# Optimization experiments

Measured on AMD Instinct MI355X. Metric: run time of the kernel, lower is better.

## Reference

```python
import jax, jax.numpy as jnp
import numpy as np

B, N, H, DK, DV = 2, 2048, 16, 128, 128
E = H * DV
EPS = 1e-6


def setup_inputs() -> dict:
    key = jax.random.key(0)
    ks = jax.random.split(key, 8)
    sc_qk = 1.0 / np.sqrt(E + H * DK)  # xavier_normal-ish std
    sc_e = 1.0 / np.sqrt(2 * E)
    d = {
        "x": jax.random.normal(ks[0], (B, N, E), jnp.float32),
        "Wq": jax.random.normal(ks[1], (H * DK, E), jnp.float32) * sc_qk,
        "bq": jnp.zeros((H * DK,), jnp.float32),
        "Wk": jax.random.normal(ks[2], (H * DK, E), jnp.float32) * sc_qk,
        "bk": jnp.zeros((H * DK,), jnp.float32),
        "Wv": jax.random.normal(ks[3], (E, E), jnp.float32) * sc_e,
        "bv": jnp.zeros((E,), jnp.float32),
        "Wg": jax.random.normal(ks[4], (E, E), jnp.float32) * sc_e,
        "bg": jnp.zeros((E,), jnp.float32),
        "Wo": jax.random.normal(ks[5], (E, E), jnp.float32) * sc_e,
        "bo": jnp.zeros((E,), jnp.float32),
        "start_idx": 0,
    }
    return d


def _retention_scan(q, k, v, decays):
    # q,k: [B,N,H,DK] (k already scaled), v: [B,N,H,DV]
    qs = jnp.moveaxis(q, 1, 0)  # [N,B,H,DK]
    ks_ = jnp.moveaxis(k, 1, 0)
    vs = jnp.moveaxis(v, 1, 0)
    dec = decays[None, :, None, None]  # [1,H,1,1]

    def step(state, qkv):
        qt, kt, vt = qkv
        # state_n = decay * state_{n-1} + k_n (x) v_n
        state = dec * state + kt[..., :, None] * vt[..., None, :]  # [B,H,DK,DV]
        ret = jnp.einsum("bhk,bhkv->bhv", qt, state)
        return state, ret

    init = jnp.zeros((q.shape[0], H, DK, DV), q.dtype)
    final_state, rets = jax.lax.scan(step, init, (qs, ks_, vs))
    return jnp.moveaxis(rets, 0, 1), final_state  # [B,N,H,DV], [B,H,DK,DV]


def reference(x, Wq, bq, Wk, bk, Wv, bv, Wg, bg, Wo, bo, start_idx):
    b, n, _ = x.shape
    decays = 1.0 - jnp.exp2(-5.0 - jnp.arange(H, dtype=jnp.float32))  # [H]
    q = (x @ Wq.T + bq).reshape(b, n, H, DK)
    k = (x @ Wk.T + bk).reshape(b, n, H, DK) / (DK ** 0.5)
    v = (x @ Wv.T + bv).reshape(b, n, H, DV)
    retention, state = _retention_scan(q, k, v, decays)
    # GroupNorm over (b n) tokens, num_groups=H, channels=E, no affine
    r = retention.reshape(b * n, H, DV).astype(jnp.float32)
    mu = jnp.mean(r, axis=-1, keepdims=True)
    var = jnp.var(r, axis=-1, keepdims=True)
    r = (r - mu) / jnp.sqrt(var + EPS)
    r = r.reshape(b, n, E).astype(x.dtype)
    gate = jax.nn.silu(x @ Wg.T + bg)
    out = (r * gate) @ Wo.T + bo
    return out, state
```

## Files before the change

kernel.cpp:

```cpp
#include <hip/hip_runtime.h>
#include <hip/hip_bf16.h>

typedef __attribute__((ext_vector_type(8))) short short8;
typedef __attribute__((ext_vector_type(4))) short short4v;
typedef __attribute__((ext_vector_type(4))) float floatx4;

#define DI __device__ __forceinline__

constexpr int B_ = 2, N_ = 2048, H_ = 16, DK_ = 128, DV_ = 128, E_ = 2048;
constexpr int M_ = B_ * N_;
constexpr int NCAT_ = 4 * E_;
constexpr int CH_ = 128;
constexpr int NC_ = N_ / CH_;
constexpr float KSCALE = 0.08838834764831845f;

constexpr long OFF_XB   = 0;
constexpr long OFF_WCAT = 16777216;
constexpr long OFF_WOB  = 50331648;
constexpr long OFF_BCAT = 58720256;
constexpr long OFF_Y    = 58753024;
constexpr long OFF_KT   = 125861888;
constexpr long OFF_VT   = 142639104;
constexpr long OFF_SCB  = 159416320;

DI unsigned short f2bf(float f){
  unsigned u = __float_as_uint(f);
  u += 0x7fffu + ((u >> 16) & 1u);
  return (unsigned short)(u >> 16);
}
DI float bf2f(unsigned short s){ return __uint_as_float(((unsigned)s) << 16); }

DI void gload_lds16(const void* g, void* l){
  __builtin_amdgcn_global_load_lds(
      (const __attribute__((address_space(1))) unsigned int*)g,
      (__attribute__((address_space(3))) unsigned int*)l, 16, 0, 0);
}

__global__ void k_cast(const float* __restrict__ s, unsigned short* __restrict__ d, int n){
  long i = ((long)blockIdx.x * blockDim.x + threadIdx.x) * 8;
  if(i >= n) return;
  float4 v0 = *(const float4*)(s + i);
  float4 v1 = *(const float4*)(s + i + 4);
  short8 o;
  o[0]=(short)f2bf(v0.x); o[1]=(short)f2bf(v0.y); o[2]=(short)f2bf(v0.z); o[3]=(short)f2bf(v0.w);
  o[4]=(short)f2bf(v1.x); o[5]=(short)f2bf(v1.y); o[6]=(short)f2bf(v1.z); o[7]=(short)f2bf(v1.w);
  *(short8*)(d + i) = o;
}

__global__ void k_bcat(const float* __restrict__ bq, const float* __restrict__ bk,
                       const float* __restrict__ bv, const float* __restrict__ bg,
                       float* __restrict__ bcat){
  int i = blockIdx.x * blockDim.x + threadIdx.x;
  float v;
  if(i < 2048)      v = bq[i];
  else if(i < 4096) v = bk[i - 2048];
  else if(i < 6144) v = bv[i - 4096];
  else              v = bg[i - 6144];
  bcat[i] = v;
}

__global__ __launch_bounds__(512, 2)
void k_gemm256(const unsigned short* __restrict__ A,
               const unsigned short* __restrict__ Bt,
               unsigned short* __restrict__ Y,
               const float* __restrict__ bias)
{
  extern __shared__ unsigned short lds[];
  constexpr int K = 2048;
  constexpr int NKT = K / 64;

  const int tid = threadIdx.x;
  const int wave = tid >> 6, lane = tid & 63;
  const int wr = wave >> 2, wc = wave & 3;
  const int l15 = lane & 15;

  int bid = blockIdx.x;
  int g = bid & 7, w = bid >> 3;
  int bm = (g & 1) * 8 + (w & 7);
  int bn = (g >> 1) * 8 + (w >> 3);

  const unsigned short* Ab = A  + (long)bm * 256 * K;
  const unsigned short* Bb = Bt + (long)bn * 256 * K;

  const int srow = wave * 8 + (lane >> 3);
  const int ce   = ((lane & 7) ^ ((lane >> 3) & 7)) * 8;

  const int colb[2] = { ((((lane >> 4))    ^ (lane & 7)) << 4),
                        ((((lane >> 4)+4)  ^ (lane & 7)) << 4) };
  int rbA[8], rbB[4];
  #pragma unroll
  for(int ai=0;ai<8;++ai) rbA[ai] = (ai>>2)*16384 + ((wr*64 + (ai&3)*16 + l15) << 7);
  #pragma unroll
  for(int bj=0;bj<4;++bj) rbB[bj] = (bj>>1)*16384 + ((wc*32 + (bj&1)*16 + l15) << 7);

  floatx4 acc[8][4] = {};
  const char* ldsc = (const char*)lds;

#define STG(op, buf, half, kt) do{                                                   \
    const unsigned short* _s = ((op) ? Bb : Ab) + (long)((half)*128 + srow)*K + (long)(kt)*64 + ce; \
    unsigned short* _d = lds + ((op)*32768 + (buf)*16384 + (half)*8192 + wave*512);  \
    gload_lds16(_s, _d);                                                             \
    gload_lds16(_s + 64*K, _d + 4096);                                               \
  }while(0)

  STG(0, 0, 0, 0);
  STG(1, 0, 0, 0);
  STG(0, 0, 1, 0);
  STG(1, 0, 1, 0);

  for(int u=0; u<NKT; ++u){
    const int cur = u & 1, nxt = cur ^ 1;
    const int ktn = (u + 1) & (NKT - 1);

    __syncthreads();

    STG(0, nxt, 0, ktn);
    STG(1, nxt, 0, ktn);
    STG(0, nxt, 1, ktn);
    STG(1, nxt, 1, ktn);

    const char* cA = ldsc + cur*32768;
    const char* cB = ldsc + 65536 + cur*32768;

    #pragma unroll
    for(int kk=0;kk<2;++kk){
      short8 a8[8], b4[4];
      #pragma unroll
      for(int ai=0;ai<8;++ai) a8[ai] = *(const short8*)(cA + rbA[ai] + colb[kk]);
      #pragma unroll
      for(int bj=0;bj<4;++bj) b4[bj] = *(const short8*)(cB + rbB[bj] + colb[kk]);
      #pragma unroll
      for(int ai=0;ai<8;++ai)
        #pragma unroll
        for(int bj=0;bj<4;++bj)
          acc[ai][bj] = __builtin_amdgcn_mfma_f32_16x16x32_bf16(a8[ai], b4[bj], acc[ai][bj], 0,0,0);
    }
  }
#undef STG

  #pragma unroll
  for(int ai=0;ai<8;++ai){
    const int rowi = bm*256 + (ai>>2)*128 + wr*64 + (ai&3)*16 + ((lane>>4)<<2);
    #pragma unroll
    for(int bj=0;bj<4;++bj){
      const int col = bn*256 + (bj>>1)*128 + wc*32 + (bj&1)*16 + l15;
      const float bs = bias[col];
      const int sec = col >> 11;
      #pragma unroll
      for(int r=0;r<4;++r){
        float v = acc[ai][bj][r] + bs;
        if(sec == 1) v *= KSCALE;
        else if(sec == 3) v = v / (1.f + __expf(-v));
        Y[(long)(rowi + r) * NCAT_ + col] = f2bf(v);
      }
    }
  }
}

template<int EPI>
__global__ __launch_bounds__(256)
void k_gemm(const unsigned short* __restrict__ A,
            const unsigned short* __restrict__ Bt,
            void* __restrict__ outp,
            const float* __restrict__ bias,
            int M, int Ncols, int K, int NB)
{
  __shared__ unsigned short lA[2*128*64];
  __shared__ unsigned short lB[2*128*64];
  const int bid = blockIdx.x;
  const int bm = bid / NB, bn = bid % NB;
  const int tid = threadIdx.x;
  const int wave = tid >> 6, lane = tid & 63;
  const int wr = wave >> 1, wc = wave & 1;

  floatx4 acc[4][4] = {};

  int srow[4], scol[4];
  #pragma unroll
  for(int is=0; is<4; ++is){
    int o = is*4096 + wave*1024 + lane*16;
    int row = o >> 7;
    int logcb = (o & 127) ^ ((row & 7) << 4);
    srow[is] = row; scol[is] = logcb >> 1;
  }
  const unsigned short* Abase = A + (long)bm * 128 * K;
  const unsigned short* Bbase = Bt + (long)bn * 128 * K;

#define STG128(kt, buf) do{                                                          \
    const int _k0 = (kt) << 6;                                                       \
    _Pragma("unroll")                                                                \
    for(int is=0; is<4; ++is){                                                       \
      gload_lds16(Abase + (long)srow[is]*K + _k0 + scol[is], &lA[(buf)*8192 + ((is*4096 + wave*1024) >> 1)]); \
      gload_lds16(Bbase + (long)srow[is]*K + _k0 + scol[is], &lB[(buf)*8192 + ((is*4096 + wave*1024) >> 1)]); \
    }                                                                                \
  }while(0)

  const int nkt = K >> 6;
  STG128(0, 0);
  for(int kt=0; kt<nkt; ++kt){
    const int cur = kt & 1, nxt = cur ^ 1;
    const int ktn = (kt + 1 == nkt) ? 0 : kt + 1;
    __syncthreads();
    STG128(ktn, nxt);
    const char* cA = (const char*)lA + cur*16384;
    const char* cB = (const char*)lB + cur*16384;
    #pragma unroll
    for(int kk=0; kk<2; ++kk){
      const int cb = (kk<<6) + ((lane>>4)<<4);
      short8 af[4], bfr[4];
      #pragma unroll
      for(int i=0;i<4;++i){
        int row = (wr<<6) + (i<<4) + (lane&15);
        af[i] = *(const short8*)(cA + (row<<7) + (cb ^ ((row&7)<<4)));
      }
      #pragma unroll
      for(int j=0;j<4;++j){
        int row = (wc<<6) + (j<<4) + (lane&15);
        bfr[j] = *(const short8*)(cB + (row<<7) + (cb ^ ((row&7)<<4)));
      }
      #pragma unroll
      for(int i=0;i<4;++i)
        #pragma unroll
        for(int j=0;j<4;++j)
          acc[i][j] = __builtin_amdgcn_mfma_f32_16x16x32_bf16(af[i], bfr[j], acc[i][j], 0,0,0);
    }
  }
#undef STG128

  #pragma unroll
  for(int i=0;i<4;++i){
    #pragma unroll
    for(int j=0;j<4;++j){
      #pragma unroll
      for(int r=0;r<4;++r){
        int row = bm*128 + (wr<<6) + (i<<4) + ((lane>>4)<<2) + r;
        int col = bn*128 + (wc<<6) + (j<<4) + (lane&15);
        float v = acc[i][j][r] + bias[col];
        if(EPI == 0){
          int sec = col >> 11;
          if(sec == 1) v *= KSCALE;
          else if(sec == 3) v = v / (1.f + __expf(-v));
          ((unsigned short*)outp)[(long)row * Ncols + col] = f2bf(v);
        } else {
          ((float*)outp)[(long)row * Ncols + col] = v;
        }
      }
    }
  }
}

__global__ __launch_bounds__(256)
void k_transpose(const unsigned short* __restrict__ Y,
                 unsigned short* __restrict__ Kt, unsigned short* __restrict__ Vt){
  __shared__ unsigned short lt[128][136];
  int bid = blockIdx.x;
  int op = bid >> 9;
  int r  = bid & 511;
  int bh = r >> 4, c = r & 15, b = bh >> 4, h = bh & 15;
  int tid = threadIdx.x;
  float dec = 1.f - exp2f(-5.f - (float)h);
  float l2d = log2f(dec);
  int sec = op ? 4096 : 2048;
  unsigned short* Dst = op ? Vt : Kt;

  #pragma unroll
  for(int p=0;p<8;++p){
    int t = p*16 + (tid>>4);
    long src = ((long)(b*N_ + c*CH_ + t)) * NCAT_ + sec + h*128 + (tid&15)*8;
    short8 v = *(const short8*)(Y + src);
    if(op == 0){
      float f = exp2f(-(float)t * l2d);
      #pragma unroll
      for(int u=0;u<8;++u) v[u] = (short)f2bf(bf2f((unsigned short)v[u]) * f);
    }
    *(short8*)&lt[t][(tid&15)*8] = v;
  }
  __syncthreads();
  #pragma unroll
  for(int p=0;p<8;++p){
    int dk = p*16 + (tid>>4);
    int tc = (tid&15)*8;
    short8 o;
    #pragma unroll
    for(int u=0;u<8;++u) o[u] = (short)lt[tc+u][dk];
    *(short8*)(Dst + ((long)(bh*128 + dk)) * N_ + c*CH_ + tc) = o;
  }
}

__global__ __launch_bounds__(256)
void k_chunksum(const unsigned short* __restrict__ Ktd, const unsigned short* __restrict__ Vt,
                float* __restrict__ MS){
  int bid = blockIdx.x;
  int bh = bid >> 4, c = bid & 15, h = bh & 15;
  int tid = threadIdx.x, wave = tid >> 6, lane = tid & 63;
  int wr = wave >> 1, wc = wave & 1;
  floatx4 acc[4][4] = {};
  const unsigned short* Vb = Vt  + (long)bh*128*N_ + c*CH_;
  const unsigned short* Kb = Ktd + (long)bh*128*N_ + c*CH_;

  #pragma unroll
  for(int kk=0;kk<4;++kk){
    int tl = kk*32 + ((lane>>4)<<3);
    short8 af[4], bfr[4];
    #pragma unroll
    for(int i=0;i<4;++i){ int dv = (wr<<6)+(i<<4)+(lane&15); af[i]  = *(const short8*)(Vb + (long)dv*N_ + tl); }
    #pragma unroll
    for(int j=0;j<4;++j){ int dk = (wc<<6)+(j<<4)+(lane&15); bfr[j] = *(const short8*)(Kb + (long)dk*N_ + tl); }
    #pragma unroll
    for(int i=0;i<4;++i)
      #pragma unroll
      for(int j=0;j<4;++j)
        acc[i][j] = __builtin_amdgcn_mfma_f32_16x16x32_bf16(af[i], bfr[j], acc[i][j], 0,0,0);
  }
  float dec = 1.f - exp2f(-5.f - (float)h);
  float scale = exp2f(127.f * log2f(dec));
  float* Mo = MS + ((long)bh*NC_ + c) * 16384;
  #pragma unroll
  for(int i=0;i<4;++i)
    #pragma unroll
    for(int j=0;j<4;++j)
      #pragma unroll
      for(int r=0;r<4;++r){
        int dv = (wr<<6)+(i<<4)+((lane>>4)<<2)+r;
        int dk = (wc<<6)+(j<<4)+(lane&15);
        Mo[dv*128 + dk] = acc[i][j][r] * scale;
      }
}

__global__ __launch_bounds__(256)
void k_scan(const float* __restrict__ MS, unsigned short* __restrict__ Scb,
            float* __restrict__ stateOut){
  int bid = blockIdx.x;
  int bh = bid >> 4, p = bid & 15;
  int tid = threadIdx.x, h = bh & 15;
  float dec = 1.f - exp2f(-5.f - (float)h);
  float decC = exp2f(128.f * log2f(dec));
  int e0 = p*1024 + tid*4;
  floatx4 S = {0.f, 0.f, 0.f, 0.f};
  const float* base = MS + (long)bh * NC_ * 16384 + e0;
  unsigned short* sb = Scb + (long)bh * NC_ * 16384 + e0;
  for(int c=0;c<NC_;++c){
    floatx4 m = *(const floatx4*)(base + (long)c*16384);
    short4v q;
    #pragma unroll
    for(int u=0;u<4;++u) q[u] = (short)f2bf(S[u]);
    *(short4v*)(sb + (long)c*16384) = q;
    S = decC * S + m;
  }
  int dv = e0 >> 7, dk = e0 & 127;
  float* so = stateOut + (long)bh*16384 + dv;
  #pragma unroll
  for(int u=0;u<4;++u) so[(long)(dk+u)*128] = S[u];
}

__global__ __launch_bounds__(256)
void k_ret(const unsigned short* __restrict__ Y, const unsigned short* __restrict__ Vt,
           const unsigned short* __restrict__ Scb, unsigned short* __restrict__ RG){
  __shared__ unsigned short sQ[128*128];
  __shared__ unsigned short sK[128*128];
  int bid = blockIdx.x;
  int bh = bid >> 4, c = bid & 15, b = bh >> 4, h = bh & 15;
  int tid = threadIdx.x, w = tid >> 6, lane = tid & 63;
  float dec = 1.f - exp2f(-5.f - (float)h);
  float l2d = log2f(dec);

  #pragma unroll
  for(int p=0;p<8;++p){
    int t = p*16 + (tid>>4);
    long row = (long)(b*N_ + c*CH_ + t) * NCAT_ + h*128 + (tid&15)*8;
    short8 qv = *(const short8*)(Y + row);
    short8 kv = *(const short8*)(Y + row + 2048);
    float fq = exp2f((float)t * l2d);
    float fk = exp2f(-(float)t * l2d);
    short8 qs, ks;
    #pragma unroll
    for(int u=0;u<8;++u){
      qs[u] = (short)f2bf(bf2f((unsigned short)qv[u]) * fq);
      ks[u] = (short)f2bf(bf2f((unsigned short)kv[u]) * fk);
    }
    int ad = t*256 + (((tid&15)*16) ^ ((t&7)<<4));
    *(short8*)((char*)sQ + ad) = qs;
    *(short8*)((char*)sK + ad) = ks;
  }
  __syncthreads();

  floatx4 acc[2][8] = {};
  #pragma unroll
  for(int kk=0;kk<4;++kk){
    int cb = (kk<<6) + ((lane>>4)<<4);
    short8 af[2], bfr[8];
    #pragma unroll
    for(int i=0;i<2;++i){ int t = w*32 + (i<<4) + (lane&15); af[i] = *(const short8*)((const char*)sQ + t*256 + (cb ^ ((t&7)<<4))); }
    #pragma unroll
    for(int j=0;j<8;++j){ int s = (j<<4) + (lane&15); bfr[j] = *(const short8*)((const char*)sK + s*256 + (cb ^ ((s&7)<<4))); }
    #pragma unroll
    for(int i=0;i<2;++i)
      #pragma unroll
      for(int j=0;j<8;++j)
        acc[i][j] = __builtin_amdgcn_mfma_f32_16x16x32_bf16(af[i], bfr[j], acc[i][j], 0,0,0);
  }
  __syncthreads();

  #pragma unroll
  for(int i=0;i<2;++i)
    #pragma unroll
    for(int j=0;j<8;++j)
      #pragma unroll
      for(int r=0;r<4;++r){
        int t = w*32 + (i<<4) + ((lane>>4)<<2) + r;
        int s = (j<<4) + (lane&15);
        float v = (s <= t) ? acc[i][j][r] : 0.f;
        *(unsigned short*)((char*)sK + t*256 + ((s*2) ^ ((t&7)<<4))) = f2bf(v);
      }
  __syncthreads();

  #pragma unroll
  for(int i=0;i<2;++i)
    #pragma unroll
    for(int j=0;j<8;++j)
      #pragma unroll
      for(int u=0;u<4;++u) acc[i][j][u] = 0.f;

  const unsigned short* Vb = Vt + (long)bh*128*N_ + c*CH_;
  #pragma unroll
  for(int kk=0;kk<4;++kk){
    int cb = (kk<<6) + ((lane>>4)<<4);
    int sg = kk*32 + ((lane>>4)<<3);
    short8 af[2], bfr[8];
    #pragma unroll
    for(int i=0;i<2;++i){ int t = w*32 + (i<<4) + (lane&15); af[i] = *(const short8*)((const char*)sK + t*256 + (cb ^ ((t&7)<<4))); }
    #pragma unroll
    for(int j=0;j<8;++j){ int dv = (j<<4) + (lane&15); bfr[j] = *(const short8*)(Vb + (long)dv*N_ + sg); }
    #pragma unroll
    for(int i=0;i<2;++i)
      #pragma unroll
      for(int j=0;j<8;++j)
        acc[i][j] = __builtin_amdgcn_mfma_f32_16x16x32_bf16(af[i], bfr[j], acc[i][j], 0,0,0);
  }
  const unsigned short* Sb = Scb + ((long)bh*NC_ + c) * 16384;
  #pragma unroll
  for(int kk=0;kk<4;++kk){
    int cb = (kk<<6) + ((lane>>4)<<4);
    int kg = kk*32 + ((lane>>4)<<3);
    short8 af[2], bfr[8];
    #pragma unroll
    for(int i=0;i<2;++i){
      int t = w*32 + (i<<4) + (lane&15);
      short8 qv = *(const short8*)((const char*)sQ + t*256 + (cb ^ ((t&7)<<4)));
      #pragma unroll
      for(int u=0;u<8;++u) af[i][u] = (short)f2bf(bf2f((unsigned short)qv[u]) * dec);
    }
    #pragma unroll
    for(int j=0;j<8;++j){ int dv = (j<<4) + (lane&15); bfr[j] = *(const short8*)(Sb + (long)dv*128 + kg); }
    #pragma unroll
    for(int i=0;i<2;++i)
      #pragma unroll
      for(int j=0;j<8;++j)
        acc[i][j] = __builtin_amdgcn_mfma_f32_16x16x32_bf16(af[i], bfr[j], acc[i][j], 0,0,0);
  }

  #pragma unroll
  for(int i=0;i<2;++i){
    #pragma unroll
    for(int r=0;r<4;++r){
      float s1 = 0.f, s2 = 0.f;
      #pragma unroll
      for(int j=0;j<8;++j){ float v = acc[i][j][r]; s1 += v; s2 += v*v; }
      #pragma unroll
      for(int off=1; off<16; off<<=1){ s1 += __shfl_xor(s1, off); s2 += __shfl_xor(s2, off); }
      float mu  = s1 * (1.f/128.f);
      float var = s2 * (1.f/128.f) - mu*mu;
      float inv = rsqrtf(var + 1e-6f);
      int t = w*32 + (i<<4) + ((lane>>4)<<2) + r;
      long mrow = (long)(b*N_ + c*CH_ + t);
      #pragma unroll
      for(int j=0;j<8;++j){
        int dv = (j<<4) + (lane&15);
        float v = (acc[i][j][r] - mu) * inv;
        float g = bf2f(Y[mrow*NCAT_ + 6144 + h*128 + dv]);
        RG[mrow*E_ + h*128 + dv] = f2bf(v * g);
      }
    }
  }
}

extern "C" void kernel_launch(void* const* d_in, const int* in_sizes, int n_in,
                              void* d_out, int out_size, void* d_ws, size_t ws_size,
                              hipStream_t stream) {
  const float* x  = (const float*)d_in[0];
  const float* Wq = (const float*)d_in[1];
  const float* bq = (const float*)d_in[2];
  const float* Wk = (const float*)d_in[3];
  const float* bk = (const float*)d_in[4];
  const float* Wv = (const float*)d_in[5];
  const float* bv = (const float*)d_in[6];
  const float* Wg = (const float*)d_in[7];
  const float* bg = (const float*)d_in[8];
  const float* Wo = (const float*)d_in[9];
  const float* bo = (const float*)d_in[10];

  char* ws = (char*)d_ws;
  unsigned short* xb   = (unsigned short*)(ws + OFF_XB);
  unsigned short* Wcat = (unsigned short*)(ws + OFF_WCAT);
  unsigned short* Wob  = (unsigned short*)(ws + OFF_WOB);
  float*          bcat = (float*)(ws + OFF_BCAT);
  unsigned short* Y    = (unsigned short*)(ws + OFF_Y);
  unsigned short* Ktd  = (unsigned short*)(ws + OFF_KT);
  unsigned short* Vt   = (unsigned short*)(ws + OFF_VT);
  unsigned short* Scb  = (unsigned short*)(ws + OFF_SCB);
  float*          MS   = (float*)(ws + OFF_WCAT);
  unsigned short* RG   = (unsigned short*)(ws + OFF_XB);

  float* outp     = (float*)d_out;
  float* stateOut = outp + (long)M_ * E_;

  (void)hipFuncSetAttribute((const void*)k_gemm256,
                            hipFuncAttributeMaxDynamicSharedMemorySize, 131072);

  k_cast<<<4096, 256, 0, stream>>>(x, xb, M_*E_);
  k_cast<<<2048, 256, 0, stream>>>(Wq, Wcat + 0L,        E_*E_);
  k_cast<<<2048, 256, 0, stream>>>(Wk, Wcat + 1L*E_*E_,  E_*E_);
  k_cast<<<2048, 256, 0, stream>>>(Wv, Wcat + 2L*E_*E_,  E_*E_);
  k_cast<<<2048, 256, 0, stream>>>(Wg, Wcat + 3L*E_*E_,  E_*E_);
  k_cast<<<2048, 256, 0, stream>>>(Wo, Wob, E_*E_);
  k_bcat<<<32, 256, 0, stream>>>(bq, bk, bv, bg, bcat);

  k_gemm256<<<512, 512, 131072, stream>>>(xb, Wcat, Y, bcat);

  k_transpose<<<1024, 256, 0, stream>>>(Y, Ktd, Vt);

  k_chunksum<<<512, 256, 0, stream>>>(Ktd, Vt, MS);
  k_scan<<<512, 256, 0, stream>>>(MS, Scb, stateOut);
  k_ret<<<512, 256, 0, stream>>>(Y, Vt, Scb, RG);

  k_gemm<1><<<(M_/128)*(E_/128), 256, 0, stream>>>(RG, Wob, (void*)outp, bo, M_, E_, E_, E_/128);
}
```

Measured before the change: 295.8 us.

## Stream B operand directly from global in QKVG GEMM and merge cast kernels

The large projection GEMM no longer stages the weight tile through LDS. Each wave now loads its B fragments straight from global memory into registers each k-step, while only A is double-buffered in LDS, which halves shared memory to 64KB. The wave layout changes from 2x4 to a row-major 128x64 per-wave tile. Separately, the six cast launches and the bias concat are merged into one kernel to cut launch overhead. The trade is that B reads are no longer shared across waves through LDS, so global/L2 traffic and load latency exposure rise.

```diff
diff --git a/kernel.cpp b/kernel.cpp
--- a/kernel.cpp
+++ b/kernel.cpp
@@ -36,27 +36,43 @@
       (__attribute__((address_space(3))) unsigned int*)l, 16, 0, 0);
 }
 
-__global__ void k_cast(const float* __restrict__ s, unsigned short* __restrict__ d, int n){
-  long i = ((long)blockIdx.x * blockDim.x + threadIdx.x) * 8;
-  if(i >= n) return;
+__global__ void k_castall(const float* __restrict__ x,
+                          const float* __restrict__ Wq, const float* __restrict__ Wk,
+                          const float* __restrict__ Wv, const float* __restrict__ Wg,
+                          const float* __restrict__ Wo,
+                          const float* __restrict__ bq, const float* __restrict__ bk,
+                          const float* __restrict__ bv, const float* __restrict__ bg,
+                          unsigned short* __restrict__ xb, unsigned short* __restrict__ Wcat,
+                          unsigned short* __restrict__ Wob, float* __restrict__ bcat){
+  int bid = blockIdx.x;
+  if(bid >= 14336){
+    int i = (bid - 14336) * 2048 + threadIdx.x * 8;
+    #pragma unroll
+    for(int u=0;u<8;++u){
+      int j = i + u;
+      float v;
+      if(j < 2048)      v = bq[j];
+      else if(j < 4096) v = bk[j - 2048];
+      else if(j < 6144) v = bv[j - 4096];
+      else              v = bg[j - 6144];
+      bcat[j] = v;
+    }
+    return;
+  }
+  const float* s; unsigned short* d; long off;
+  if(bid < 4096){ s = x; d = xb; off = (long)bid*2048; }
+  else if(bid < 6144){ s = Wq; d = Wcat;            off = (long)(bid-4096)*2048; }
+  else if(bid < 8192){ s = Wk; d = Wcat + 4194304L; off = (long)(bid-6144)*2048; }
+  else if(bid < 10240){ s = Wv; d = Wcat + 8388608L; off = (long)(bid-8192)*2048; }
+  else if(bid < 12288){ s = Wg; d = Wcat + 12582912L; off = (long)(bid-10240)*2048; }
+  else { s = Wo; d = Wob; off = (long)(bid-12288)*2048; }
+  long i = off + (long)threadIdx.x * 8;
   float4 v0 = *(const float4*)(s + i);
   float4 v1 = *(const float4*)(s + i + 4);
   short8 o;
   o[0]=(short)f2bf(v0.x); o[1]=(short)f2bf(v0.y); o[2]=(short)f2bf(v0.z); o[3]=(short)f2bf(v0.w);
   o[4]=(short)f2bf(v1.x); o[5]=(short)f2bf(v1.y); o[6]=(short)f2bf(v1.z); o[7]=(short)f2bf(v1.w);
   *(short8*)(d + i) = o;
-}
-
-__global__ void k_bcat(const float* __restrict__ bq, const float* __restrict__ bk,
-                       const float* __restrict__ bv, const float* __restrict__ bg,
-                       float* __restrict__ bcat){
-  int i = blockIdx.x * blockDim.x + threadIdx.x;
-  float v;
-  if(i < 2048)      v = bq[i];
-  else if(i < 4096) v = bk[i - 2048];
-  else if(i < 6144) v = bv[i - 4096];
-  else              v = bg[i - 6144];
-  bcat[i] = v;
 }
 
 __global__ __launch_bounds__(512, 2)
@@ -80,70 +96,70 @@
   int bn = (g >> 1) * 8 + (w >> 3);
 
   const unsigned short* Ab = A  + (long)bm * 256 * K;
-  const unsigned short* Bb = Bt + (long)bn * 256 * K;
-
-  const int srow = wave * 8 + (lane >> 3);
-  const int ce   = ((lane & 7) ^ ((lane >> 3) & 7)) * 8;
-
-  const int colb[2] = { ((((lane >> 4))    ^ (lane & 7)) << 4),
-                        ((((lane >> 4)+4)  ^ (lane & 7)) << 4) };
-  int rbA[8], rbB[4];
-  #pragma unroll
-  for(int ai=0;ai<8;++ai) rbA[ai] = (ai>>2)*16384 + ((wr*64 + (ai&3)*16 + l15) << 7);
-  #pragma unroll
-  for(int bj=0;bj<4;++bj) rbB[bj] = (bj>>1)*16384 + ((wc*32 + (bj&1)*16 + l15) << 7);
+
+  const int sr = (lane >> 3);
+  const int sc = ((lane & 7) ^ sr) * 8;
+  int rbA[8];
+  #pragma unroll
+  for(int ai=0;ai<8;++ai) rbA[ai] = (wr*128 + ai*16 + l15) << 7;
+  const int colx[2] = { ((0 + (lane>>4)) ^ (lane&7)) << 4,
+                        ((4 + (lane>>4)) ^ (lane&7)) << 4 };
+
+  const unsigned short* Bp = Bt + (long)(bn*256 + wc*64 + l15) * K + ((lane >> 4) << 3);
 
   floatx4 acc[8][4] = {};
   const char* ldsc = (const char*)lds;
 
-#define STG(op, buf, half, kt) do{                                                   \
-    const unsigned short* _s = ((op) ? Bb : Ab) + (long)((half)*128 + srow)*K + (long)(kt)*64 + ce; \
-    unsigned short* _d = lds + ((op)*32768 + (buf)*16384 + (half)*8192 + wave*512);  \
-    gload_lds16(_s, _d);                                                             \
-    gload_lds16(_s + 64*K, _d + 4096);                                               \
+#define STG_A(buf, kt) do{                                                            \
+    _Pragma("unroll")                                                                 \
+    for(int s=0;s<4;++s){                                                             \
+      const int _i = wave*4 + s;                                                      \
+      gload_lds16(Ab + (long)(_i*8 + sr)*K + (long)(kt)*64 + sc,                      \
+                  &lds[(buf)*16384 + _i*512 + lane*8]);                               \
+    }                                                                                 \
   }while(0)
 
-  STG(0, 0, 0, 0);
-  STG(1, 0, 0, 0);
-  STG(0, 0, 1, 0);
-  STG(1, 0, 1, 0);
+  STG_A(0, 0);
 
   for(int u=0; u<NKT; ++u){
     const int cur = u & 1, nxt = cur ^ 1;
     const int ktn = (u + 1) & (NKT - 1);
 
     __syncthreads();
-
-    STG(0, nxt, 0, ktn);
-    STG(1, nxt, 0, ktn);
-    STG(0, nxt, 1, ktn);
-    STG(1, nxt, 1, ktn);
+    STG_A(nxt, ktn);
+
+    short8 b0[4], b1[4];
+    {
+      const unsigned short* Bk = Bp + (long)u * 64;
+      #pragma unroll
+      for(int bj=0;bj<4;++bj){
+        b0[bj] = *(const short8*)(Bk + (long)bj*16*K);
+        b1[bj] = *(const short8*)(Bk + (long)bj*16*K + 32);
+      }
+    }
 
     const char* cA = ldsc + cur*32768;
-    const char* cB = ldsc + 65536 + cur*32768;
-
     #pragma unroll
     for(int kk=0;kk<2;++kk){
-      short8 a8[8], b4[4];
-      #pragma unroll
-      for(int ai=0;ai<8;++ai) a8[ai] = *(const short8*)(cA + rbA[ai] + colb[kk]);
-      #pragma unroll
-      for(int bj=0;bj<4;++bj) b4[bj] = *(const short8*)(cB + rbB[bj] + colb[kk]);
+      short8 a8[8];
+      #pragma unroll
+      for(int ai=0;ai<8;++ai) a8[ai] = *(const short8*)(cA + rbA[ai] + colx[kk]);
       #pragma unroll
       for(int ai=0;ai<8;++ai)
         #pragma unroll
         for(int bj=0;bj<4;++bj)
-          acc[ai][bj] = __builtin_amdgcn_mfma_f32_16x16x32_bf16(a8[ai], b4[bj], acc[ai][bj], 0,0,0);
-    }
-  }
-#undef STG
+          acc[ai][bj] = __builtin_amdgcn_mfma_f32_16x16x32_bf16(
+              a8[ai], kk ? b1[bj] : b0[bj], acc[ai][bj], 0,0,0);
+    }
+  }
+#undef STG_A
 
   #pragma unroll
   for(int ai=0;ai<8;++ai){
-    const int rowi = bm*256 + (ai>>2)*128 + wr*64 + (ai&3)*16 + ((lane>>4)<<2);
+    const int rowi = bm*256 + wr*128 + ai*16 + ((lane>>4)<<2);
     #pragma unroll
     for(int bj=0;bj<4;++bj){
-      const int col = bn*256 + (bj>>1)*128 + wc*32 + (bj&1)*16 + l15;
+      const int col = bn*256 + wc*64 + bj*16 + l15;
       const float bs = bias[col];
       const int sec = col >> 11;
       #pragma unroll
@@ -515,17 +531,12 @@
   float* stateOut = outp + (long)M_ * E_;
 
   (void)hipFuncSetAttribute((const void*)k_gemm256,
-                            hipFuncAttributeMaxDynamicSharedMemorySize, 131072);
-
-  k_cast<<<4096, 256, 0, stream>>>(x, xb, M_*E_);
-  k_cast<<<2048, 256, 0, stream>>>(Wq, Wcat + 0L,        E_*E_);
-  k_cast<<<2048, 256, 0, stream>>>(Wk, Wcat + 1L*E_*E_,  E_*E_);
-  k_cast<<<2048, 256, 0, stream>>>(Wv, Wcat + 2L*E_*E_,  E_*E_);
-  k_cast<<<2048, 256, 0, stream>>>(Wg, Wcat + 3L*E_*E_,  E_*E_);
-  k_cast<<<2048, 256, 0, stream>>>(Wo, Wob, E_*E_);
-  k_bcat<<<32, 256, 0, stream>>>(bq, bk, bv, bg, bcat);
-
-  k_gemm256<<<512, 512, 131072, stream>>>(xb, Wcat, Y, bcat);
+                            hipFuncAttributeMaxDynamicSharedMemorySize, 65536);
+
+  k_castall<<<14340, 256, 0, stream>>>(x, Wq, Wk, Wv, Wg, Wo, bq, bk, bv, bg,
+                                       xb, Wcat, Wob, bcat);
+
+  k_gemm256<<<512, 512, 65536, stream>>>(xb, Wcat, Y, bcat);
 
   k_transpose<<<1024, 256, 0, stream>>>(Y, Ktd, Vt);
 
```

After: 360.2 us. +21.8%, slower.
